# Kernel tuning notes

Hardware: AMD Instinct MI355X
Metric: run time of the kernel (lower is better)

The kernel has to match this reference:

```python
import jax, jax.numpy as jnp
import numpy as np

HIDDEN = 1024
VOCAB = 50257


def setup_inputs() -> dict:
    key = jax.random.key(0)
    ks = jax.random.split(key, 9)
    s = 0.02
    return {
        "token": jax.random.randint(ks[0], (1,), 0, VOCAB, dtype=jnp.int64),
        "hidden": jax.random.normal(ks[1], (1, 1, HIDDEN), dtype=jnp.float32),
        "emb": jax.random.normal(ks[2], (VOCAB, HIDDEN), dtype=jnp.float32) * s,
        "w_ih": jax.random.normal(ks[3], (3 * HIDDEN, HIDDEN), dtype=jnp.float32) * s,
        "w_hh": jax.random.normal(ks[4], (3 * HIDDEN, HIDDEN), dtype=jnp.float32) * s,
        "b_ih": jax.random.normal(ks[5], (3 * HIDDEN,), dtype=jnp.float32) * s,
        "b_hh": jax.random.normal(ks[6], (3 * HIDDEN,), dtype=jnp.float32) * s,
        "w_out": jax.random.normal(ks[7], (VOCAB, HIDDEN), dtype=jnp.float32) * s,
        "b_out": jax.random.normal(ks[8], (VOCAB,), dtype=jnp.float32) * s,
    }


def reference(token, hidden, emb, w_ih, w_hh, b_ih, b_hh, w_out, b_out):
    # embed + relu: [1, H]
    x = jax.nn.relu(emb[token].reshape(1, HIDDEN))
    h = hidden[0]  # [1, H]
    # single-step GRU (PyTorch gate order r, z, n; separate biases)
    gi = x @ w_ih.T + b_ih  # [1, 3H]
    gh = h @ w_hh.T + b_hh  # [1, 3H]
    i_r, i_z, i_n = jnp.split(gi, 3, axis=-1)
    h_r, h_z, h_n = jnp.split(gh, 3, axis=-1)
    r = jax.nn.sigmoid(i_r + h_r)
    z = jax.nn.sigmoid(i_z + h_z)
    n = jnp.tanh(i_n + r * h_n)
    h_new = (1.0 - z) * n + z * h  # [1, H]
    # output projection + log-softmax over vocab
    logits = h_new @ w_out.T + b_out  # [1, V]
    logp = jax.nn.log_softmax(logits, axis=1)
    return logp, h_new[None]  # ([1, V], [1, 1, H])
```

## Files before the change

### kernel.cpp

```cpp
#include <hip/hip_runtime.h>
#include <math.h>

#define HIDDEN 1024
#define VOCAB 50257
#define K2_BLOCKS 1024
#define NW (K2_BLOCKS * 4)

__device__ __forceinline__ float wave_reduce_sum(float v) {
#pragma unroll
    for (int m = 1; m < 64; m <<= 1) v += __shfl_xor(v, m, 64);
    return v;
}

__global__ __launch_bounds__(192) void gru_kernel(
    const int* token_p, const float* __restrict__ hidden, const float* __restrict__ emb,
    const float* __restrict__ w_ih, const float* __restrict__ w_hh,
    const float* __restrict__ b_ih, const float* __restrict__ b_hh,
    float* __restrict__ h_new_out, float* __restrict__ h_new_ws) {
    const int g = threadIdx.x >> 6;
    const int lane = threadIdx.x & 63;
    const int j = blockIdx.x;

    const int token = token_p[0];
    const float4* x4 = (const float4*)(emb + (size_t)token * HIDDEN);
    const float4* h4 = (const float4*)hidden;
    const float4* wi = (const float4*)(w_ih + (size_t)(g * HIDDEN + j) * HIDDEN);
    const float4* wh = (const float4*)(w_hh + (size_t)(g * HIDDEN + j) * HIDDEN);

    float acc_i = 0.f, acc_h = 0.f;
#pragma unroll
    for (int k = 0; k < 4; ++k) {
        const int idx = k * 64 + lane;
        float4 e = x4[idx];
        float4 h = h4[idx];
        float4 a = wi[idx];
        float4 b = wh[idx];
        e.x = fmaxf(e.x, 0.f); e.y = fmaxf(e.y, 0.f);
        e.z = fmaxf(e.z, 0.f); e.w = fmaxf(e.w, 0.f);
        acc_i += a.x * e.x + a.y * e.y + a.z * e.z + a.w * e.w;
        acc_h += b.x * h.x + b.y * h.y + b.z * h.z + b.w * h.w;
    }
    acc_i = wave_reduce_sum(acc_i);
    acc_h = wave_reduce_sum(acc_h);

    __shared__ float red_i[3], red_h[3];
    if (lane == 0) { red_i[g] = acc_i; red_h[g] = acc_h; }
    __syncthreads();

    if (threadIdx.x == 0) {
        const float i_r = red_i[0] + b_ih[j];
        const float i_z = red_i[1] + b_ih[HIDDEN + j];
        const float i_n = red_i[2] + b_ih[2 * HIDDEN + j];
        const float h_r = red_h[0] + b_hh[j];
        const float h_z = red_h[1] + b_hh[HIDDEN + j];
        const float h_n = red_h[2] + b_hh[2 * HIDDEN + j];
        const float r = 1.f / (1.f + expf(-(i_r + h_r)));
        const float z = 1.f / (1.f + expf(-(i_z + h_z)));
        const float n = tanhf(i_n + r * h_n);
        const float hv = (1.f - z) * n + z * hidden[j];
        h_new_out[j] = hv;
        h_new_ws[j] = hv;
    }
}

__global__ __launch_bounds__(256) void logits_kernel(
    const float* __restrict__ h_new, const float* __restrict__ w_out,
    const float* __restrict__ b_out, float* __restrict__ logits,
    float* __restrict__ partials) {
    const int wave = threadIdx.x >> 6;
    const int lane = threadIdx.x & 63;
    const int gw = blockIdx.x * 4 + wave;

    const float4* h4 = (const float4*)h_new;
    float4 hs[4];
#pragma unroll
    for (int k = 0; k < 4; ++k) hs[k] = h4[k * 64 + lane];

    float m = -INFINITY, s = 0.f;
    for (int v = gw; v < VOCAB; v += 2 * NW) {
        const int v2 = v + NW;
        const bool has2 = (v2 < VOCAB);
        const float4* w1 = (const float4*)(w_out + (size_t)v * HIDDEN);
        const float4* w2 = (const float4*)(w_out + (size_t)(has2 ? v2 : v) * HIDDEN);
        float a1 = 0.f, a2 = 0.f;
#pragma unroll
        for (int k = 0; k < 4; ++k) {
            const int idx = k * 64 + lane;
            float4 x = w1[idx];
            float4 y = w2[idx];
            a1 += x.x * hs[k].x + x.y * hs[k].y + x.z * hs[k].z + x.w * hs[k].w;
            a2 += y.x * hs[k].x + y.y * hs[k].y + y.z * hs[k].z + y.w * hs[k].w;
        }
        a1 = wave_reduce_sum(a1);
        a2 = wave_reduce_sum(a2);

        const float l1 = a1 + b_out[v];
        if (lane == 0) logits[v] = l1;
        if (l1 > m) { s *= expf(m - l1); m = l1; }
        s += expf(l1 - m);

        if (has2) {
            const float l2 = a2 + b_out[v2];
            if (lane == 0) logits[v2] = l2;
            if (l2 > m) { s *= expf(m - l2); m = l2; }
            s += expf(l2 - m);
        }
    }

    __shared__ float sm[4], ss[4];
    if (lane == 0) { sm[wave] = m; ss[wave] = s; }
    __syncthreads();
    if (threadIdx.x == 0) {
        float M = fmaxf(fmaxf(sm[0], sm[1]), fmaxf(sm[2], sm[3]));
        float S = ss[0] * expf(sm[0] - M) + ss[1] * expf(sm[1] - M) +
                  ss[2] * expf(sm[2] - M) + ss[3] * expf(sm[3] - M);
        partials[2 * blockIdx.x] = M;
        partials[2 * blockIdx.x + 1] = S;
    }
}

__global__ __launch_bounds__(256) void finalize_kernel(
    const float* __restrict__ partials, float* __restrict__ logits) {
    const int t = threadIdx.x;
    const int wave = t >> 6;
    const int lane = t & 63;

    float m = -INFINITY, s = 0.f;
#pragma unroll
    for (int i = 0; i < K2_BLOCKS / 256; ++i) {
        const int idx = i * 256 + t;
        const float pm = partials[2 * idx];
        const float ps = partials[2 * idx + 1];
        const float M = fmaxf(m, pm);
        s = s * expf(m - M) + ps * expf(pm - M);
        m = M;
    }
#pragma unroll
    for (int o = 1; o < 64; o <<= 1) {
        const float pm = __shfl_xor(m, o, 64);
        const float ps = __shfl_xor(s, o, 64);
        const float M = fmaxf(m, pm);
        s = s * expf(m - M) + ps * expf(pm - M);
        m = M;
    }
    __shared__ float sm[4], ss[4];
    if (lane == 0) { sm[wave] = m; ss[wave] = s; }
    __syncthreads();
    const float M = fmaxf(fmaxf(sm[0], sm[1]), fmaxf(sm[2], sm[3]));
    const float S = ss[0] * expf(sm[0] - M) + ss[1] * expf(sm[1] - M) +
                    ss[2] * expf(sm[2] - M) + ss[3] * expf(sm[3] - M);
    const float c = M + logf(S);

    float4* l4 = (float4*)logits;
    const int n4 = VOCAB / 4;
    for (int i = blockIdx.x * 256 + t; i < n4; i += gridDim.x * 256) {
        float4 x = l4[i];
        x.x -= c; x.y -= c; x.z -= c; x.w -= c;
        l4[i] = x;
    }
    if (blockIdx.x == 0 && t == 0) logits[VOCAB - 1] -= c;
}

extern "C" void kernel_launch(void* const* d_in, const int* in_sizes, int n_in,
                              void* d_out, int out_size, void* d_ws, size_t ws_size,
                              hipStream_t stream) {
    const int*   token  = (const int*)d_in[0];
    const float* hidden = (const float*)d_in[1];
    const float* emb    = (const float*)d_in[2];
    const float* w_ih   = (const float*)d_in[3];
    const float* w_hh   = (const float*)d_in[4];
    const float* b_ih   = (const float*)d_in[5];
    const float* b_hh   = (const float*)d_in[6];
    const float* w_out  = (const float*)d_in[7];
    const float* b_out  = (const float*)d_in[8];

    float* out      = (float*)d_out;
    float* h_new    = out + VOCAB;
    float* logits   = out;
    float* ws       = (float*)d_ws;
    float* partials = ws;
    float* h_new_ws = ws + 2 * K2_BLOCKS;

    gru_kernel<<<HIDDEN, 192, 0, stream>>>(token, hidden, emb, w_ih, w_hh,
                                           b_ih, b_hh, h_new, h_new_ws);
    logits_kernel<<<K2_BLOCKS, 256, 0, stream>>>(h_new_ws, w_out, b_out, logits,
                                                 partials);
    finalize_kernel<<<64, 256, 0, stream>>>(partials, logits);
}
```

Measured before the change: 45.97 us.

## Double logits grid and assign contiguous vocab ranges per wave

Doubles the number of blocks in the logits kernel and gives each wave a contiguous, evenly balanced range of vocab rows instead of strided rows. Rows are processed in pairs with a single rescale of the online softmax per pair, and a tail handles an odd leftover row. The aim is more memory parallelism and better load balance across waves; the finalize kernel now reduces twice as many partials.

```diff
diff --git a/kernel.cpp b/kernel.cpp
--- a/kernel.cpp
+++ b/kernel.cpp
@@ -3,7 +3,7 @@
 
 #define HIDDEN 1024
 #define VOCAB 50257
-#define K2_BLOCKS 1024
+#define K2_BLOCKS 2048
 #define NW (K2_BLOCKS * 4)
 
 __device__ __forceinline__ float wave_reduce_sum(float v) {
@@ -71,17 +71,21 @@
     const int lane = threadIdx.x & 63;
     const int gw = blockIdx.x * 4 + wave;
 
+    const int BASE = VOCAB / NW;
+    const int EXTRA = VOCAB - BASE * NW;
+    const int start = gw * BASE + (gw < EXTRA ? gw : EXTRA);
+    const int end = start + BASE + (gw < EXTRA ? 1 : 0);
+
     const float4* h4 = (const float4*)h_new;
     float4 hs[4];
 #pragma unroll
     for (int k = 0; k < 4; ++k) hs[k] = h4[k * 64 + lane];
 
     float m = -INFINITY, s = 0.f;
-    for (int v = gw; v < VOCAB; v += 2 * NW) {
-        const int v2 = v + NW;
-        const bool has2 = (v2 < VOCAB);
+    int v = start;
+    for (; v + 1 < end; v += 2) {
         const float4* w1 = (const float4*)(w_out + (size_t)v * HIDDEN);
-        const float4* w2 = (const float4*)(w_out + (size_t)(has2 ? v2 : v) * HIDDEN);
+        const float4* w2 = (const float4*)(w_out + (size_t)(v + 1) * HIDDEN);
         float a1 = 0.f, a2 = 0.f;
 #pragma unroll
         for (int k = 0; k < 4; ++k) {
@@ -95,16 +99,26 @@
         a2 = wave_reduce_sum(a2);
 
         const float l1 = a1 + b_out[v];
+        const float l2 = a2 + b_out[v + 1];
+        if (lane == 0) { logits[v] = l1; logits[v + 1] = l2; }
+        const float mx = fmaxf(l1, l2);
+        if (mx > m) { s *= expf(m - mx); m = mx; }
+        s += expf(l1 - m) + expf(l2 - m);
+    }
+    if (v < end) {
+        const float4* w1 = (const float4*)(w_out + (size_t)v * HIDDEN);
+        float a1 = 0.f;
+#pragma unroll
+        for (int k = 0; k < 4; ++k) {
+            const int idx = k * 64 + lane;
+            float4 x = w1[idx];
+            a1 += x.x * hs[k].x + x.y * hs[k].y + x.z * hs[k].z + x.w * hs[k].w;
+        }
+        a1 = wave_reduce_sum(a1);
+        const float l1 = a1 + b_out[v];
         if (lane == 0) logits[v] = l1;
         if (l1 > m) { s *= expf(m - l1); m = l1; }
         s += expf(l1 - m);
-
-        if (has2) {
-            const float l2 = a2 + b_out[v2];
-            if (lane == 0) logits[v2] = l2;
-            if (l2 > m) { s *= expf(m - l2); m = l2; }
-            s += expf(l2 - m);
-        }
     }
 
     __shared__ float sm[4], ss[4];
```

Result: no change. 45.21 us (median of 2 runs) (-1.7%).
